# Optimization experiments

Hardware: AMD Instinct MI355X
Metric: run time of the kernel (lower is better)

## Reference

```python
import jax, jax.numpy as jnp
import numpy as np

C = 256          # hidden_size
H = 8            # num_heads
HD = C // H      # head dim = 32
W = 8            # window side; N = W*W = 64 tokens per window
N = W * W
NW = 64          # windows per image
B = 32           # images
B_ = B * NW      # 2048


def make_rel_index():
    # identical to the torch buffer construction (meshgrid 'ij')
    coords = np.stack(np.meshgrid(np.arange(W), np.arange(W), indexing='ij'))  # (2,W,W)
    flat = coords.reshape(2, -1)                       # (2, N)
    rel = flat[:, :, None] - flat[:, None, :]          # (2, N, N)
    rel = rel.transpose(1, 2, 0).astype(np.int64)      # (N, N, 2)
    rel[..., 0] += W - 1
    rel[..., 1] += W - 1
    rel[..., 0] *= 2 * W - 1
    return jnp.asarray(rel.sum(-1), jnp.int32)         # (N, N) in [0, 225)


def setup_inputs() -> dict:
    key = jax.random.key(0)
    ks = jax.random.split(key, 12)
    x = jax.random.normal(ks[0], (B_, N, C), jnp.float32)
    # Swin-style additive mask: 0 for allowed, -1e9 for masked pairs
    keep = jax.random.uniform(ks[1], (NW, N, N)) > 0.1
    mask = jnp.where(keep, 0.0, -1e9).astype(jnp.float32)
    std = 0.02
    wq = jax.random.normal(ks[2], (C, C), jnp.float32) * std
    bq = jnp.zeros((C,), jnp.float32)
    wk = jax.random.normal(ks[3], (C, C), jnp.float32) * std
    bk = jnp.zeros((C,), jnp.float32)
    wv = jax.random.normal(ks[4], (C, C), jnp.float32) * std
    bv = jnp.zeros((C,), jnp.float32)
    wp = jax.random.normal(ks[5], (C, C), jnp.float32) * std
    bp = jnp.zeros((C,), jnp.float32)
    bias_table = jax.random.normal(ks[6], ((2 * W - 1) ** 2, H), jnp.float32) * std
    rel_index = make_rel_index()
    return {"x": x, "mask": mask, "wq": wq, "bq": bq, "wk": wk, "bk": bk,
            "wv": wv, "bv": bv, "wp": wp, "bp": bp,
            "bias_table": bias_table, "rel_index": rel_index}


def reference(x, mask, wq, bq, wk, bk, wv, bv, wp, bp, bias_table, rel_index):
    B_, N, C = x.shape
    nW = mask.shape[0]
    H = bias_table.shape[1]
    HD = C // H
    scale = HD ** -0.5

    def heads(t):  # (B_, N, C) -> (B_, H, N, HD)
        return t.reshape(B_, N, H, HD).transpose(0, 2, 1, 3)

    q = heads(x @ wq + bq) * scale
    k = heads(x @ wk + bk)
    v = heads(x @ wv + bv)

    attn = jnp.einsum('bhnd,bhmd->bhnm', q, k)            # (B_, H, N, N)
    bias = bias_table[rel_index]                          # (N, N, H)
    attn = attn + bias.transpose(2, 0, 1)[None]           # + (1, H, N, N)
    # add per-window shift mask, broadcast over batch and heads
    attn = attn.reshape(B_ // nW, nW, H, N, N) + mask[None, :, None]
    attn = jax.nn.softmax(attn.reshape(B_, H, N, N), axis=-1)

    out = jnp.einsum('bhnm,bhmd->bhnd', attn, v)          # (B_, H, N, HD)
    out = out.transpose(0, 2, 1, 3).reshape(B_, N, C)
    return out @ wp + bp
```

## Files before the change

kernel.cpp:

```cpp
#include <hip/hip_runtime.h>
#include <hip/hip_bf16.h>

typedef __bf16 bf16;
typedef __bf16 bf16x4 __attribute__((ext_vector_type(4)));
typedef __bf16 bf16x8 __attribute__((ext_vector_type(8)));
typedef float  f32x4  __attribute__((ext_vector_type(4)));
typedef short  s16x4  __attribute__((ext_vector_type(4)));

#define DEVI __device__ __forceinline__

static constexpr float kScale = 0.17677669529663687f;

DEVI f32x4 mfma32(bf16x8 a, bf16x8 b, f32x4 c) {
  return __builtin_amdgcn_mfma_f32_16x16x32_bf16(a, b, c, 0, 0, 0);
}
DEVI f32x4 mfma16(bf16x4 a, bf16x4 b, f32x4 c) {
#if __has_builtin(__builtin_amdgcn_mfma_f32_16x16x16bf16_1k)
  return __builtin_amdgcn_mfma_f32_16x16x16bf16_1k(
      __builtin_bit_cast(s16x4, a), __builtin_bit_cast(s16x4, b), c, 0, 0, 0);
#else
  f32x4 d;
  asm volatile("v_mfma_f32_16x16x16_bf16 %0, %1, %2, %3"
               : "=v"(d)
               : "v"(a), "v"(b), "v"(c));
  return d;
#endif
}
DEVI bf16x4 pk4(f32x4 v) {
  bf16x4 p;
  p[0] = (bf16)v[0]; p[1] = (bf16)v[1]; p[2] = (bf16)v[2]; p[3] = (bf16)v[3];
  return p;
}

DEVI const bf16x8* wfp(const char* base, int fi, int w, int nt, int lane) {
  return (const bf16x8*)(base + (((size_t)fi * 16 + w * 4 + nt) * 64 + lane) * 16);
}

__global__ __launch_bounds__(256) void prep_kernel(
    const float* __restrict__ wq, const float* __restrict__ bq,
    const float* __restrict__ wk, const float* __restrict__ bk,
    const float* __restrict__ wv, const float* __restrict__ bv,
    const float* __restrict__ wp,
    const float* __restrict__ bias_table, const int* __restrict__ rel_index,
    const float* __restrict__ mask,
    char* __restrict__ wstream, char* __restrict__ wpstream,
    float* __restrict__ bqkv, bf16* __restrict__ biasM) {
  int idx = blockIdx.x * 256 + threadIdx.x;
  if (idx < 196608) {
    int m = idx >> 16, n = idx & 255, k = (idx >> 8) & 255;
    const float* w = (m == 0) ? wq : (m == 1 ? wk : wv);
    float v = w[k * 256 + n];
    if (m == 0) v *= kScale;
    int fi = m * 8 + (k >> 5);
    int wv_ = n >> 6, nt = (n >> 4) & 3;
    int lane = ((k >> 3) & 3) * 16 + (n & 15);
    *(bf16*)(wstream + (((size_t)fi * 16 + wv_ * 4 + nt) * 64 + lane) * 16 +
             (k & 7) * 2) = (bf16)v;
  } else if (idx < 262144) {
    int rem = idx - 196608;
    int n = rem & 255, k = (rem >> 8) & 255;
    int fi = k >> 5;
    int wv_ = n >> 6, nt = (n >> 4) & 3;
    int lane = ((k >> 3) & 3) * 16 + (n & 15);
    *(bf16*)(wpstream + (((size_t)fi * 16 + wv_ * 4 + nt) * 64 + lane) * 16 +
             (k & 7) * 2) = (bf16)wp[k * 256 + n];
  } else if (idx < 262912) {
    int rem = idx - 262144;
    int m = rem >> 8, n = rem & 255;
    const float* b = (m == 0) ? bq : (m == 1 ? bk : bv);
    float v = b[n];
    if (m == 0) v *= kScale;
    bqkv[rem] = v;
  } else if (idx < 2360064) {
    int rem = idx - 262912;
    int w = rem >> 15, h = (rem >> 12) & 7, ij = rem & 4095;
    biasM[rem] = (bf16)(bias_table[rel_index[ij] * 8 + h] + mask[w * 4096 + ij]);
  }
}

__global__ __launch_bounds__(256, 2) void swin_kernel(
    const float* __restrict__ x, const char* __restrict__ wstream,
    const char* __restrict__ wpstream, const float* __restrict__ bqkv,
    const float* __restrict__ bp, const bf16* __restrict__ biasM,
    float* __restrict__ out) {
  __shared__ __align__(16) char xs_ob[32768];

  int tid = threadIdx.x;
  int w = tid >> 6, lane = tid & 63;
  int g = lane >> 4, c = lane & 15;
  int bid = blockIdx.x;
  int win = (bid & 7) * 256 + ((bid >> 3) & 3) * 64 + (bid >> 5);
  const f32x4 fz = {0.f, 0.f, 0.f, 0.f};

  {
    const char* xw = (const char*)(x + (size_t)win * 16384);
#pragma unroll
    for (int i = 0; i < 8; ++i) {
      int gb = i * 8192 + tid * 32;
      float4 f0 = *(const float4*)(xw + gb);
      float4 f1 = *(const float4*)(xw + gb + 16);
      bf16x8 v;
      v[0] = (bf16)f0.x; v[1] = (bf16)f0.y; v[2] = (bf16)f0.z; v[3] = (bf16)f0.w;
      v[4] = (bf16)f1.x; v[5] = (bf16)f1.y; v[6] = (bf16)f1.z; v[7] = (bf16)f1.w;
      int t = gb >> 10, ir = (gb & 1023) >> 1;
      *(bf16x8*)(xs_ob + ((t * 512 + ir) ^ ((t & 7) << 4))) = v;
    }
  }
  __syncthreads();

  bf16x4 qp[4][4], kp[4][4], vp[4][4];

  {
    f32x4 acc[4][4];
#pragma unroll
    for (int nt = 0; nt < 4; ++nt) {
      f32x4 b4 = *(const f32x4*)(bqkv + 0 * 256 + w * 64 + nt * 16 + g * 4);
#pragma unroll
      for (int tt = 0; tt < 4; ++tt) acc[tt][nt] = b4;
    }
#pragma unroll
    for (int kq = 0; kq < 8; ++kq) {
      bf16x8 wf[4], xf[4];
#pragma unroll
      for (int nt = 0; nt < 4; ++nt) wf[nt] = *wfp(wstream, kq, w, nt, lane);
#pragma unroll
      for (int tt = 0; tt < 4; ++tt)
        xf[tt] = *(const bf16x8*)(
            xs_ob + (((tt * 16 + c) * 512 + kq * 64 + g * 16) ^ ((c & 7) << 4)));
#pragma unroll
      for (int tt = 0; tt < 4; ++tt)
#pragma unroll
        for (int nt = 0; nt < 4; ++nt)
          acc[tt][nt] = mfma32(wf[nt], xf[tt], acc[tt][nt]);
    }
#pragma unroll
    for (int tt = 0; tt < 4; ++tt)
#pragma unroll
      for (int nt = 0; nt < 4; ++nt) qp[tt][nt] = pk4(acc[tt][nt]);
  }
  {
    f32x4 acc[4][4];
#pragma unroll
    for (int nt = 0; nt < 4; ++nt) {
      f32x4 b4 = *(const f32x4*)(bqkv + 1 * 256 + w * 64 + nt * 16 + g * 4);
#pragma unroll
      for (int tt = 0; tt < 4; ++tt) acc[tt][nt] = b4;
    }
#pragma unroll
    for (int kq = 0; kq < 8; ++kq) {
      bf16x8 wf[4], xf[4];
#pragma unroll
      for (int nt = 0; nt < 4; ++nt) wf[nt] = *wfp(wstream, 8 + kq, w, nt, lane);
#pragma unroll
      for (int tt = 0; tt < 4; ++tt)
        xf[tt] = *(const bf16x8*)(
            xs_ob + (((tt * 16 + c) * 512 + kq * 64 + g * 16) ^ ((c & 7) << 4)));
#pragma unroll
      for (int tt = 0; tt < 4; ++tt)
#pragma unroll
        for (int nt = 0; nt < 4; ++nt)
          acc[tt][nt] = mfma32(wf[nt], xf[tt], acc[tt][nt]);
    }
#pragma unroll
    for (int tt = 0; tt < 4; ++tt)
#pragma unroll
      for (int nt = 0; nt < 4; ++nt) kp[tt][nt] = pk4(acc[tt][nt]);
  }
  {
    f32x4 acc[4][4];
#pragma unroll
    for (int nt = 0; nt < 4; ++nt) {
      float bv_ = bqkv[512 + w * 64 + nt * 16 + c];
      f32x4 b4 = {bv_, bv_, bv_, bv_};
#pragma unroll
      for (int tt = 0; tt < 4; ++tt) acc[tt][nt] = b4;
    }
#pragma unroll
    for (int kq = 0; kq < 8; ++kq) {
      bf16x8 wf[4], xf[4];
#pragma unroll
      for (int nt = 0; nt < 4; ++nt) wf[nt] = *wfp(wstream, 16 + kq, w, nt, lane);
#pragma unroll
      for (int tt = 0; tt < 4; ++tt)
        xf[tt] = *(const bf16x8*)(
            xs_ob + (((tt * 16 + c) * 512 + kq * 64 + g * 16) ^ ((c & 7) << 4)));
#pragma unroll
      for (int tt = 0; tt < 4; ++tt)
#pragma unroll
        for (int nt = 0; nt < 4; ++nt)
          acc[tt][nt] = mfma32(xf[tt], wf[nt], acc[tt][nt]);
    }
#pragma unroll
    for (int tt = 0; tt < 4; ++tt)
#pragma unroll
      for (int nt = 0; nt < 4; ++nt) vp[tt][nt] = pk4(acc[tt][nt]);
  }
  __syncthreads();

#pragma unroll
  for (int hh = 0; hh < 2; ++hh) {
    int h = w * 2 + hh;
    const bf16* bm = biasM + ((size_t)(win & 63) * 8 + h) * 4096;
#pragma unroll
    for (int mi = 0; mi < 4; ++mi) {
      f32x4 s[4];
#pragma unroll
      for (int mj = 0; mj < 4; ++mj) {
        bf16x4 b4 = *(const bf16x4*)(bm + (mi * 16 + c) * 64 + mj * 16 + g * 4);
        s[mj] = (f32x4){(float)b4[0], (float)b4[1], (float)b4[2], (float)b4[3]};
      }
#pragma unroll
      for (int dd = 0; dd < 2; ++dd)
#pragma unroll
        for (int mj = 0; mj < 4; ++mj)
          s[mj] = mfma16(kp[mj][hh * 2 + dd], qp[mi][hh * 2 + dd], s[mj]);
      float mx;
      {
        f32x4 m4 = s[0];
#pragma unroll
        for (int mj = 1; mj < 4; ++mj) {
          m4[0] = fmaxf(m4[0], s[mj][0]); m4[1] = fmaxf(m4[1], s[mj][1]);
          m4[2] = fmaxf(m4[2], s[mj][2]); m4[3] = fmaxf(m4[3], s[mj][3]);
        }
        mx = fmaxf(fmaxf(m4[0], m4[1]), fmaxf(m4[2], m4[3]));
        mx = fmaxf(mx, __shfl_xor(mx, 16));
        mx = fmaxf(mx, __shfl_xor(mx, 32));
      }
      float sum;
      {
        f32x4 s4 = fz;
#pragma unroll
        for (int mj = 0; mj < 4; ++mj) {
#pragma unroll
          for (int r = 0; r < 4; ++r) s[mj][r] = __expf(s[mj][r] - mx);
          s4 += s[mj];
        }
        sum = (s4[0] + s4[1]) + (s4[2] + s4[3]);
        sum += __shfl_xor(sum, 16);
        sum += __shfl_xor(sum, 32);
      }
      float rs = 1.0f / sum;
      bf16x4 pf[4];
#pragma unroll
      for (int mj = 0; mj < 4; ++mj) pf[mj] = pk4(s[mj]);
#pragma unroll
      for (int dt = 0; dt < 2; ++dt) {
        f32x4 o = fz;
#pragma unroll
        for (int mj = 0; mj < 4; ++mj)
          o = mfma16(vp[mj][hh * 2 + dt], pf[mj], o);
        bf16x4 ov;
        ov[0] = (bf16)(o[0] * rs); ov[1] = (bf16)(o[1] * rs);
        ov[2] = (bf16)(o[2] * rs); ov[3] = (bf16)(o[3] * rs);
        *(bf16x4*)(xs_ob + (((mi * 16 + c) * 512 + (h * 32 + dt * 16 + g * 4) * 2) ^
                            ((c & 7) << 4))) = ov;
      }
    }
  }
  __syncthreads();

  f32x4 acc2[4][4];
#pragma unroll
  for (int nt = 0; nt < 4; ++nt) {
    f32x4 b4 = *(const f32x4*)(bp + w * 64 + nt * 16 + g * 4);
#pragma unroll
    for (int tt = 0; tt < 4; ++tt) acc2[tt][nt] = b4;
  }
#pragma unroll
  for (int kq = 0; kq < 8; ++kq) {
    bf16x8 wf[4], of[4];
#pragma unroll
    for (int nt = 0; nt < 4; ++nt) wf[nt] = *wfp(wpstream, kq, w, nt, lane);
#pragma unroll
    for (int tt = 0; tt < 4; ++tt)
      of[tt] = *(const bf16x8*)(
          xs_ob + (((tt * 16 + c) * 512 + kq * 64 + g * 16) ^ ((c & 7) << 4)));
#pragma unroll
    for (int tt = 0; tt < 4; ++tt)
#pragma unroll
      for (int nt = 0; nt < 4; ++nt)
        acc2[tt][nt] = mfma32(wf[nt], of[tt], acc2[tt][nt]);
  }
#pragma unroll
  for (int tt = 0; tt < 4; ++tt)
#pragma unroll
    for (int nt = 0; nt < 4; ++nt)
      *(f32x4*)(out + ((size_t)win * 64 + tt * 16 + c) * 256 + w * 64 + nt * 16 + g * 4) =
          acc2[tt][nt];
}

extern "C" void kernel_launch(void* const* d_in, const int* in_sizes, int n_in,
                              void* d_out, int out_size, void* d_ws, size_t ws_size,
                              hipStream_t stream) {
  const float* x          = (const float*)d_in[0];
  const float* mask       = (const float*)d_in[1];
  const float* wq         = (const float*)d_in[2];
  const float* bq         = (const float*)d_in[3];
  const float* wk         = (const float*)d_in[4];
  const float* bk         = (const float*)d_in[5];
  const float* wv         = (const float*)d_in[6];
  const float* bv         = (const float*)d_in[7];
  const float* wp         = (const float*)d_in[8];
  const float* bp         = (const float*)d_in[9];
  const float* bias_table = (const float*)d_in[10];
  const int*   rel_index  = (const int*)d_in[11];

  char* ws = (char*)d_ws;
  size_t o = 0;
  char* wstream = ws + o;  o += (size_t)24 * 16384;
  char* wpstream = ws + o; o += (size_t)8 * 16384;
  float* bqkv = (float*)(ws + o); o += (size_t)768 * 4;
  bf16* biasM = (bf16*)(ws + o); o += (size_t)64 * 8 * 64 * 64 * 2;
  if (ws_size < o) return;

  prep_kernel<<<9219, 256, 0, stream>>>(wq, bq, wk, bk, wv, bv, wp,
                                        bias_table, rel_index, mask,
                                        wstream, wpstream, bqkv, biasM);
  swin_kernel<<<2048, 256, 0, stream>>>(x, wstream, wpstream, bqkv, bp, biasM,
                                        (float*)d_out);
}
```

Baseline: 192.1 us.

## Split QKV projection into half-width passes and raise occupancy to three blocks

Result: slower. 610.4 us (+217.8%).

```diff
diff --git a/kernel.cpp b/kernel.cpp
--- a/kernel.cpp
+++ b/kernel.cpp
@@ -78,7 +78,7 @@
   }
 }
 
-__global__ __launch_bounds__(256, 2) void swin_kernel(
+__global__ __launch_bounds__(256, 3) void swin_kernel(
     const float* __restrict__ x, const char* __restrict__ wstream,
     const char* __restrict__ wpstream, const float* __restrict__ bqkv,
     const float* __restrict__ bp, const bf16* __restrict__ biasM,
@@ -88,8 +88,7 @@
   int tid = threadIdx.x;
   int w = tid >> 6, lane = tid & 63;
   int g = lane >> 4, c = lane & 15;
-  int bid = blockIdx.x;
-  int win = (bid & 7) * 256 + ((bid >> 3) & 3) * 64 + (bid >> 5);
+  int win = blockIdx.x;
   const f32x4 fz = {0.f, 0.f, 0.f, 0.f};
 
   {
@@ -110,90 +109,61 @@
 
   bf16x4 qp[4][4], kp[4][4], vp[4][4];
 
-  {
-    f32x4 acc[4][4];
-#pragma unroll
-    for (int nt = 0; nt < 4; ++nt) {
-      f32x4 b4 = *(const f32x4*)(bqkv + 0 * 256 + w * 64 + nt * 16 + g * 4);
-#pragma unroll
-      for (int tt = 0; tt < 4; ++tt) acc[tt][nt] = b4;
+#pragma unroll
+  for (int m = 0; m < 3; ++m) {
+#pragma unroll
+    for (int h2 = 0; h2 < 2; ++h2) {
+      f32x4 acc[4][2];
+      if (m < 2) {
+#pragma unroll
+        for (int n2 = 0; n2 < 2; ++n2) {
+          f32x4 b4 = *(const f32x4*)(bqkv + m * 256 + w * 64 + (h2 * 2 + n2) * 16 + g * 4);
+#pragma unroll
+          for (int tt = 0; tt < 4; ++tt) acc[tt][n2] = b4;
+        }
+      } else {
+#pragma unroll
+        for (int n2 = 0; n2 < 2; ++n2) {
+          float bv_ = bqkv[512 + w * 64 + (h2 * 2 + n2) * 16 + c];
+          f32x4 b4 = {bv_, bv_, bv_, bv_};
+#pragma unroll
+          for (int tt = 0; tt < 4; ++tt) acc[tt][n2] = b4;
+        }
+      }
+#pragma unroll
+      for (int kq = 0; kq < 8; ++kq) {
+        bf16x8 wf[2], xf[4];
+#pragma unroll
+        for (int n2 = 0; n2 < 2; ++n2)
+          wf[n2] = *wfp(wstream, m * 8 + kq, w, h2 * 2 + n2, lane);
+#pragma unroll
+        for (int tt = 0; tt < 4; ++tt)
+          xf[tt] = *(const bf16x8*)(
+              xs_ob + (((tt * 16 + c) * 512 + kq * 64 + g * 16) ^ ((c & 7) << 4)));
+        if (m < 2) {
+#pragma unroll
+          for (int tt = 0; tt < 4; ++tt)
+#pragma unroll
+            for (int n2 = 0; n2 < 2; ++n2)
+              acc[tt][n2] = mfma32(wf[n2], xf[tt], acc[tt][n2]);
+        } else {
+#pragma unroll
+          for (int tt = 0; tt < 4; ++tt)
+#pragma unroll
+            for (int n2 = 0; n2 < 2; ++n2)
+              acc[tt][n2] = mfma32(xf[tt], wf[n2], acc[tt][n2]);
+        }
+      }
+#pragma unroll
+      for (int tt = 0; tt < 4; ++tt)
+#pragma unroll
+        for (int n2 = 0; n2 < 2; ++n2) {
+          int nt = h2 * 2 + n2;
+          if (m == 0)      qp[tt][nt] = pk4(acc[tt][n2]);
+          else if (m == 1) kp[tt][nt] = pk4(acc[tt][n2]);
+          else             vp[tt][nt] = pk4(acc[tt][n2]);
+        }
     }
-#pragma unroll
-    for (int kq = 0; kq < 8; ++kq) {
-      bf16x8 wf[4], xf[4];
-#pragma unroll
-      for (int nt = 0; nt < 4; ++nt) wf[nt] = *wfp(wstream, kq, w, nt, lane);
-#pragma unroll
-      for (int tt = 0; tt < 4; ++tt)
-        xf[tt] = *(const bf16x8*)(
-            xs_ob + (((tt * 16 + c) * 512 + kq * 64 + g * 16) ^ ((c & 7) << 4)));
-#pragma unroll
-      for (int tt = 0; tt < 4; ++tt)
-#pragma unroll
-        for (int nt = 0; nt < 4; ++nt)
-          acc[tt][nt] = mfma32(wf[nt], xf[tt], acc[tt][nt]);
-    }
-#pragma unroll
-    for (int tt = 0; tt < 4; ++tt)
-#pragma unroll
-      for (int nt = 0; nt < 4; ++nt) qp[tt][nt] = pk4(acc[tt][nt]);
-  }
-  {
-    f32x4 acc[4][4];
-#pragma unroll
-    for (int nt = 0; nt < 4; ++nt) {
-      f32x4 b4 = *(const f32x4*)(bqkv + 1 * 256 + w * 64 + nt * 16 + g * 4);
-#pragma unroll
-      for (int tt = 0; tt < 4; ++tt) acc[tt][nt] = b4;
-    }
-#pragma unroll
-    for (int kq = 0; kq < 8; ++kq) {
-      bf16x8 wf[4], xf[4];
-#pragma unroll
-      for (int nt = 0; nt < 4; ++nt) wf[nt] = *wfp(wstream, 8 + kq, w, nt, lane);
-#pragma unroll
-      for (int tt = 0; tt < 4; ++tt)
-        xf[tt] = *(const bf16x8*)(
-            xs_ob + (((tt * 16 + c) * 512 + kq * 64 + g * 16) ^ ((c & 7) << 4)));
-#pragma unroll
-      for (int tt = 0; tt < 4; ++tt)
-#pragma unroll
-        for (int nt = 0; nt < 4; ++nt)
-          acc[tt][nt] = mfma32(wf[nt], xf[tt], acc[tt][nt]);
-    }
-#pragma unroll
-    for (int tt = 0; tt < 4; ++tt)
-#pragma unroll
-      for (int nt = 0; nt < 4; ++nt) kp[tt][nt] = pk4(acc[tt][nt]);
-  }
-  {
-    f32x4 acc[4][4];
-#pragma unroll
-    for (int nt = 0; nt < 4; ++nt) {
-      float bv_ = bqkv[512 + w * 64 + nt * 16 + c];
-      f32x4 b4 = {bv_, bv_, bv_, bv_};
-#pragma unroll
-      for (int tt = 0; tt < 4; ++tt) acc[tt][nt] = b4;
-    }
-#pragma unroll
-    for (int kq = 0; kq < 8; ++kq) {
-      bf16x8 wf[4], xf[4];
-#pragma unroll
-      for (int nt = 0; nt < 4; ++nt) wf[nt] = *wfp(wstream, 16 + kq, w, nt, lane);
-#pragma unroll
-      for (int tt = 0; tt < 4; ++tt)
-        xf[tt] = *(const bf16x8*)(
-            xs_ob + (((tt * 16 + c) * 512 + kq * 64 + g * 16) ^ ((c & 7) << 4)));
-#pragma unroll
-      for (int tt = 0; tt < 4; ++tt)
-#pragma unroll
-        for (int nt = 0; nt < 4; ++nt)
-          acc[tt][nt] = mfma32(xf[tt], wf[nt], acc[tt][nt]);
-    }
-#pragma unroll
-    for (int tt = 0; tt < 4; ++tt)
-#pragma unroll
-      for (int nt = 0; nt < 4; ++nt) vp[tt][nt] = pk4(acc[tt][nt]);
   }
   __syncthreads();
 
```
